# Kernel optimization log

Measured on AMD Instinct MI355X. Metric: run time of the kernel, lower is better.

## Reference

```python
import jax, jax.numpy as jnp
import numpy as np

# PyTorch bicubic (a=-0.75), half-pixel coords, scale factor 2 -> fixed fractional
# offset t=0.5 for every output pixel, giving constant taps at src offsets [-1,0,1,2].
CUBIC_W = np.array([-0.09375, 0.59375, 0.59375, -0.09375], dtype=np.float32)


def _down_last(x):
    """Bicubic 2x downsample along the last axis (PyTorch semantics, border clamp)."""
    n = x.shape[-1]
    no = n // 2
    idx = jnp.clip(2 * jnp.arange(no)[:, None] + jnp.arange(-1, 3)[None, :], 0, n - 1)  # (no,4)
    g = x[..., idx]  # (..., no, 4)
    return jnp.einsum('...ok,k->...o', g, jnp.asarray(CUBIC_W, dtype=x.dtype))


def _downsample_bicubic(x):
    # separable: width then height (order irrelevant)
    x = _down_last(x)
    x = jnp.swapaxes(x, -1, -2)
    x = _down_last(x)
    return jnp.swapaxes(x, -1, -2)


def _fftpack_hilbert(x):
    """scipy.fftpack.hilbert: y_j = 1j*sign(j)*x_j in Fourier space, Nyquist zeroed."""
    n = x.shape[0]
    X = np.fft.fft(x)
    sgn = np.zeros(n)
    sgn[1:n // 2] = 1.0
    sgn[n // 2 + 1:] = -1.0
    return np.real(np.fft.ifft(1j * sgn * X))


def _db8_filters():
    gl = np.array([-0.00011747678400228192, 0.0006754494059985568, -0.0003917403729959771,
                   -0.00487035299301066, 0.008746094047015655, 0.013981027917015516,
                   -0.04408825393106472, -0.01736930100202211, 0.128747426620186,
                   0.00047248457399797254, -0.2840155429624281, -0.015829105256023893,
                   0.5853546836548691, 0.6756307362980128, 0.3128715909144659,
                   0.05441584224308161])
    gh = np.array([-0.05441584224308161, 0.3128715909144659, -0.6756307362980128,
                   0.5853546836548691, 0.015829105256023893, -0.2840155429624281,
                   -0.00047248457399797254, 0.128747426620186, 0.01736930100202211,
                   -0.04408825393106472, -0.013981027917015516, 0.008746094047015655,
                   0.00487035299301066, -0.0003917403729959771, -0.0006754494059985568,
                   -0.00011747678400228192])
    fl = _fftpack_hilbert(gl)
    fh = _fftpack_hilbert(gh)
    return gl, gh, fl, fh


def setup_inputs() -> dict:
    key = jax.random.key(0)
    image = jax.random.normal(key, (4, 16, 512, 512), dtype=jnp.float32)
    gl, gh, fl, fh = _db8_filters()
    return {
        'image': image,
        'gl': jnp.asarray(gl, dtype=jnp.float32),
        'gh': jnp.asarray(gh, dtype=jnp.float32),
        'fl': jnp.asarray(fl, dtype=jnp.float32),
        'fh': jnp.asarray(fh, dtype=jnp.float32),
    }


def reference(image, gl, gh, fl, fh):
    # The original _column_convolve/_row_convolve never shift X (out += X*h[idx]),
    # so after the reflect-pad gather and centered slice, colfilter/rowfilter
    # reduce exactly to X * sum(h). Each sub-band is therefore
    # downsample(image) * sum(col_filter) * sum(row_filter).
    sg, sh = jnp.sum(gl), jnp.sum(gh)
    sfl, sfh = jnp.sum(fl), jnp.sum(fh)
    D = _downsample_bicubic(image)  # (B, C, H/2, W/2)
    LL = jnp.concatenate([D * (sg * sg), D * (sfl * sg), D * (sg * sfl), D * (sfl * sfl)], axis=1)
    b1 = jnp.concatenate([D * (sg * sh), D * (sfl * sh), D * (sg * sfh), D * (sfl * sfh)], axis=1)
    b2 = jnp.concatenate([D * (sh * sg), D * (sfh * sg), D * (sh * sfl), D * (sfh * sfl)], axis=1)
    b3 = jnp.concatenate([D * (sh * sh), D * (sfh * sh), D * (sh * sfh), D * (sfh * sfh)], axis=1)
    H = jnp.stack([b1, b2, b3], axis=2)  # (B, 4C, 3, H/2, W/2)
    return (LL, H)
```

## Files before the change

### kernel.cpp

```cpp
#include <hip/hip_runtime.h>

typedef float f32x4 __attribute__((ext_vector_type(4)));

__global__ void qwt_sums_kernel(const float* __restrict__ gl, const float* __restrict__ gh,
                                const float* __restrict__ fl, const float* __restrict__ fh,
                                float* __restrict__ ws) {
    int t = threadIdx.x;
    if (t < 4) {
        const float* p = (t == 0) ? gl : (t == 1) ? gh : (t == 2) ? fl : fh;
        float s = 0.f;
        #pragma unroll
        for (int i = 0; i < 16; i++) s += p[i];
        ws[t] = s;
    }
}

__global__ __launch_bounds__(256) void qwt_main_kernel(const float* __restrict__ img,
                                                       const float* __restrict__ ws,
                                                       float* __restrict__ out) {
    const float w0 = -0.09375f, w1 = 0.59375f;

    int t    = blockIdx.x * 256 + threadIdx.x;
    int lane = t & 63;
    int wid  = t >> 6;
    int ygrp = wid & 63;
    int bc   = wid >> 6;
    int y0   = ygrp << 2;
    int x0   = lane << 2;

    float sg = ws[0], sh = ws[1], sfl = ws[2], sfh = ws[3];

    const float* src = img + (size_t)bc * (512 * 512);

    float h[10][4];
    #pragma unroll
    for (int k = 0; k < 10; k++) {
        int sr = 2 * y0 - 1 + k;
        sr = sr < 0 ? 0 : (sr > 511 ? 511 : sr);
        const f32x4* rp4 = (const f32x4*)(src + (size_t)sr * 512);
        f32x4 v0 = rp4[2 * lane];
        f32x4 v1 = rp4[2 * lane + 1];
        float left  = __shfl_up(v1.w, 1);
        float right = __shfl_down(v0.x, 1);
        if (lane == 0)  left  = v0.x;
        if (lane == 63) right = v1.w;

        h[k][0] = w0 * left + w1 * v0.x + w1 * v0.y + w0 * v0.z;
        h[k][1] = w0 * v0.y + w1 * v0.z + w1 * v0.w + w0 * v1.x;
        h[k][2] = w0 * v0.w + w1 * v1.x + w1 * v1.y + w0 * v1.z;
        h[k][3] = w0 * v1.y + w1 * v1.z + w1 * v1.w + w0 * right;
    }

    f32x4 acc[4];
    #pragma unroll
    for (int r = 0; r < 4; r++) {
        #pragma unroll
        for (int i = 0; i < 4; i++) {
            float a = w0 * h[2 * r][i] + w1 * h[2 * r + 1][i]
                    + w1 * h[2 * r + 2][i] + w0 * h[2 * r + 3][i];
            acc[r][i] = a;
        }
    }

    int b   = bc >> 4;
    int cc_ = bc & 15;
    size_t rowoff = ((size_t)y0 << 8) + (size_t)x0;
    const size_t P  = 65536;
    const size_t HB = 16777216;

    float* llp = out + ((size_t)(b * 64 + cc_)) * P + rowoff;
    float* hp  = out + HB + ((size_t)(b * 64 + cc_)) * 3 * P + rowoff;

    #pragma unroll
    for (int q = 0; q < 4; q++) {
        float f1g = (q & 1) ? sfl : sg;
        float f1h = (q & 1) ? sfh : sh;
        float f2g = (q & 2) ? sfl : sg;
        float f2h = (q & 2) ? sfh : sh;

        float sLL = f1g * f2g;
        float s0  = f1g * f2h;
        float s1  = f1h * f2g;
        float s2  = f1h * f2h;

        #pragma unroll
        for (int r = 0; r < 4; r++) {
            f32x4 v = {acc[r][0] * sLL, acc[r][1] * sLL, acc[r][2] * sLL, acc[r][3] * sLL};
            *(f32x4*)(llp + r * 256) = v;
        }
        #pragma unroll
        for (int r = 0; r < 4; r++) {
            f32x4 v = {acc[r][0] * s0, acc[r][1] * s0, acc[r][2] * s0, acc[r][3] * s0};
            *(f32x4*)(hp + r * 256) = v;
        }
        #pragma unroll
        for (int r = 0; r < 4; r++) {
            f32x4 v = {acc[r][0] * s1, acc[r][1] * s1, acc[r][2] * s1, acc[r][3] * s1};
            *(f32x4*)(hp + P + r * 256) = v;
        }
        #pragma unroll
        for (int r = 0; r < 4; r++) {
            f32x4 v = {acc[r][0] * s2, acc[r][1] * s2, acc[r][2] * s2, acc[r][3] * s2};
            *(f32x4*)(hp + 2 * P + r * 256) = v;
        }

        llp += 16 * P;
        hp  += 48 * P;
    }
}

extern "C" void kernel_launch(void* const* d_in, const int* in_sizes, int n_in,
                              void* d_out, int out_size, void* d_ws, size_t ws_size,
                              hipStream_t stream) {
    const float* img = (const float*)d_in[0];
    const float* gl  = (const float*)d_in[1];
    const float* gh  = (const float*)d_in[2];
    const float* fl  = (const float*)d_in[3];
    const float* fh  = (const float*)d_in[4];
    float* out = (float*)d_out;
    float* ws  = (float*)d_ws;

    qwt_sums_kernel<<<1, 64, 0, stream>>>(gl, gh, fl, fh, ws);
    qwt_main_kernel<<<1024, 256, 0, stream>>>(img, ws, out);
}
```

Measured before the change: 327.0 us.

## Split quadrant outputs across more blocks, fuse filter sums, use nontemporal stores

```diff
diff --git a/kernel.cpp b/kernel.cpp
--- a/kernel.cpp
+++ b/kernel.cpp
@@ -2,33 +2,33 @@
 
 typedef float f32x4 __attribute__((ext_vector_type(4)));
 
-__global__ void qwt_sums_kernel(const float* __restrict__ gl, const float* __restrict__ gh,
-                                const float* __restrict__ fl, const float* __restrict__ fh,
-                                float* __restrict__ ws) {
-    int t = threadIdx.x;
-    if (t < 4) {
-        const float* p = (t == 0) ? gl : (t == 1) ? gh : (t == 2) ? fl : fh;
-        float s = 0.f;
-        #pragma unroll
-        for (int i = 0; i < 16; i++) s += p[i];
-        ws[t] = s;
-    }
-}
-
 __global__ __launch_bounds__(256) void qwt_main_kernel(const float* __restrict__ img,
-                                                       const float* __restrict__ ws,
+                                                       const float* __restrict__ gl,
+                                                       const float* __restrict__ gh,
+                                                       const float* __restrict__ fl,
+                                                       const float* __restrict__ fh,
                                                        float* __restrict__ out) {
     const float w0 = -0.09375f, w1 = 0.59375f;
 
     int t    = blockIdx.x * 256 + threadIdx.x;
     int lane = t & 63;
     int wid  = t >> 6;
+    int q    = wid >> 12;
+    int bc   = (wid >> 6) & 63;
     int ygrp = wid & 63;
-    int bc   = wid >> 6;
     int y0   = ygrp << 2;
     int x0   = lane << 2;
 
-    float sg = ws[0], sh = ws[1], sfl = ws[2], sfh = ws[3];
+    float s = 0.f;
+    if (lane < 4) {
+        const float* p = (lane == 0) ? gl : (lane == 1) ? gh : (lane == 2) ? fl : fh;
+        #pragma unroll
+        for (int i = 0; i < 16; i++) s += p[i];
+    }
+    float sg  = __shfl(s, 0);
+    float sh  = __shfl(s, 1);
+    float sfl = __shfl(s, 2);
+    float sfh = __shfl(s, 3);
 
     const float* src = img + (size_t)bc * (512 * 512);
 
@@ -56,11 +56,19 @@
     for (int r = 0; r < 4; r++) {
         #pragma unroll
         for (int i = 0; i < 4; i++) {
-            float a = w0 * h[2 * r][i] + w1 * h[2 * r + 1][i]
-                    + w1 * h[2 * r + 2][i] + w0 * h[2 * r + 3][i];
-            acc[r][i] = a;
+            acc[r][i] = w0 * h[2 * r][i] + w1 * h[2 * r + 1][i]
+                      + w1 * h[2 * r + 2][i] + w0 * h[2 * r + 3][i];
         }
     }
+
+    float f1g = (q & 1) ? sfl : sg;
+    float f1h = (q & 1) ? sfh : sh;
+    float f2g = (q & 2) ? sfl : sg;
+    float f2h = (q & 2) ? sfh : sh;
+    float sLL = f1g * f2g;
+    float s0  = f1g * f2h;
+    float s1  = f1h * f2g;
+    float s2  = f1h * f2h;
 
     int b   = bc >> 4;
     int cc_ = bc & 15;
@@ -68,44 +76,29 @@
     const size_t P  = 65536;
     const size_t HB = 16777216;
 
-    float* llp = out + ((size_t)(b * 64 + cc_)) * P + rowoff;
-    float* hp  = out + HB + ((size_t)(b * 64 + cc_)) * 3 * P + rowoff;
+    size_t chan = (size_t)(b * 64 + q * 16 + cc_);
+    float* llp = out + chan * P + rowoff;
+    float* hp  = out + HB + chan * 3 * P + rowoff;
 
     #pragma unroll
-    for (int q = 0; q < 4; q++) {
-        float f1g = (q & 1) ? sfl : sg;
-        float f1h = (q & 1) ? sfh : sh;
-        float f2g = (q & 2) ? sfl : sg;
-        float f2h = (q & 2) ? sfh : sh;
-
-        float sLL = f1g * f2g;
-        float s0  = f1g * f2h;
-        float s1  = f1h * f2g;
-        float s2  = f1h * f2h;
-
-        #pragma unroll
-        for (int r = 0; r < 4; r++) {
-            f32x4 v = {acc[r][0] * sLL, acc[r][1] * sLL, acc[r][2] * sLL, acc[r][3] * sLL};
-            *(f32x4*)(llp + r * 256) = v;
-        }
-        #pragma unroll
-        for (int r = 0; r < 4; r++) {
-            f32x4 v = {acc[r][0] * s0, acc[r][1] * s0, acc[r][2] * s0, acc[r][3] * s0};
-            *(f32x4*)(hp + r * 256) = v;
-        }
-        #pragma unroll
-        for (int r = 0; r < 4; r++) {
-            f32x4 v = {acc[r][0] * s1, acc[r][1] * s1, acc[r][2] * s1, acc[r][3] * s1};
-            *(f32x4*)(hp + P + r * 256) = v;
-        }
-        #pragma unroll
-        for (int r = 0; r < 4; r++) {
-            f32x4 v = {acc[r][0] * s2, acc[r][1] * s2, acc[r][2] * s2, acc[r][3] * s2};
-            *(f32x4*)(hp + 2 * P + r * 256) = v;
-        }
-
-        llp += 16 * P;
-        hp  += 48 * P;
+    for (int r = 0; r < 4; r++) {
+        f32x4 v = {acc[r][0] * sLL, acc[r][1] * sLL, acc[r][2] * sLL, acc[r][3] * sLL};
+        __builtin_nontemporal_store(v, (f32x4*)(llp + r * 256));
+    }
+    #pragma unroll
+    for (int r = 0; r < 4; r++) {
+        f32x4 v = {acc[r][0] * s0, acc[r][1] * s0, acc[r][2] * s0, acc[r][3] * s0};
+        __builtin_nontemporal_store(v, (f32x4*)(hp + r * 256));
+    }
+    #pragma unroll
+    for (int r = 0; r < 4; r++) {
+        f32x4 v = {acc[r][0] * s1, acc[r][1] * s1, acc[r][2] * s1, acc[r][3] * s1};
+        __builtin_nontemporal_store(v, (f32x4*)(hp + P + r * 256));
+    }
+    #pragma unroll
+    for (int r = 0; r < 4; r++) {
+        f32x4 v = {acc[r][0] * s2, acc[r][1] * s2, acc[r][2] * s2, acc[r][3] * s2};
+        __builtin_nontemporal_store(v, (f32x4*)(hp + 2 * P + r * 256));
     }
 }
 
@@ -118,8 +111,6 @@
     const float* fl  = (const float*)d_in[3];
     const float* fh  = (const float*)d_in[4];
     float* out = (float*)d_out;
-    float* ws  = (float*)d_ws;
 
-    qwt_sums_kernel<<<1, 64, 0, stream>>>(gl, gh, fl, fh, ws);
-    qwt_main_kernel<<<1024, 256, 0, stream>>>(img, ws, out);
+    qwt_main_kernel<<<4096, 256, 0, stream>>>(img, gl, gh, fl, fh, out);
 }
```

Result: slower. 335.8 us (+2.7%).
